# Kernel tuning notes

Hardware: AMD Instinct MI355X
Metric: run time of the kernel (lower is better)

## Reference

```python
import jax, jax.numpy as jnp
import numpy as np
import math

D, DK, DV = 1024, 128, 128
B, S = 4, 2048

def setup_inputs() -> dict:
    key = jax.random.key(0)
    k1, k2, k3, k4 = jax.random.split(key, 4)
    # xavier_normal std = sqrt(2/(fan_in+fan_out))
    std_qk = math.sqrt(2.0 / (D + DK))
    std_v = math.sqrt(2.0 / (D + DV))
    return {
        "X": jax.random.normal(k1, (B, S, D), dtype=jnp.float32),
        "W_q": jax.random.normal(k2, (D, DK), dtype=jnp.float32) * std_qk,
        "W_k": jax.random.normal(k3, (D, DK), dtype=jnp.float32) * std_qk,
        "W_v": jax.random.normal(k4, (D, DV), dtype=jnp.float32) * std_v,
    }

def reference(X, W_q, W_k, W_v):
    # Q,K,V projections: [B,S,D] @ [D,dk] -> [B,S,dk]
    Q = X @ W_q
    K = X @ W_k
    V = X @ W_v
    scale = 1.0 / math.sqrt(DK)
    # NOTE: original torch code calls A.masked_fill(...) without assigning the
    # result, so the causal mask is never actually applied. We replicate the
    # executed math: unmasked scaled dot-product attention.
    A = jnp.einsum("bqd,bkd->bqk", Q, K) * scale  # [B,S,S]
    A = jax.nn.softmax(A, axis=2)
    return jnp.einsum("bqk,bkv->bqv", A, V)  # [B,S,DV]
```

## Files before the change

kernel.cpp:

```cpp
#include <hip/hip_runtime.h>
#include <stdint.h>
#include <math.h>


typedef __attribute__((ext_vector_type(4))) float  f32x4;
typedef __attribute__((ext_vector_type(4))) short  s16x4;
typedef __attribute__((ext_vector_type(8))) short  s16x8;
typedef __attribute__((ext_vector_type(4))) float  fl4;

#define MFMA(a,b,c) __builtin_amdgcn_mfma_f32_16x16x16bf16_1k(a,b,c,0,0,0)

__device__ __forceinline__ short f2bf(float f){
  uint32_t u = __builtin_bit_cast(uint32_t, f);
  u = (u + 0x7FFFu + ((u >> 16) & 1u)) >> 16;
  return (short)u;
}

#define S_LEN   2048
#define D_IN    1024
#define D_HEAD  128
#define NROWS   8192
#define NSPLIT  4
#define KVB     32
#define QBLK    64

#define WT_OFF  0u
#define Q_OFF   786432u
#define K_OFF   (786432u + 2097152u)
#define V_OFF   (786432u + 2u*2097152u)
#define OP_OFF  (786432u + 3u*2097152u)
#define ML_OFF  (OP_OFF + 16777216u)

__global__ __launch_bounds__(256) void wt3_kernel(
    const float* __restrict__ Wq, const float* __restrict__ Wk,
    const float* __restrict__ Wv, short* __restrict__ Wt){
  int i = blockIdx.x * 256 + threadIdx.x;
  int m = i >> 17;
  int r = i & 131071;
  int n = r >> 10;
  int k = r & 1023;
  const float* W = (m == 0) ? Wq : (m == 1 ? Wk : Wv);
  Wt[i] = f2bf(W[k * D_HEAD + n]);
}

__global__ __launch_bounds__(256) void proj_kernel(
    const float* __restrict__ X, const short* __restrict__ Wt,
    short* __restrict__ Qo, short* __restrict__ Ko, short* __restrict__ Vt){
  const int mt  = blockIdx.x;
  const int mat = blockIdx.y;
  const short* Wm = Wt + mat * 131072;

  __shared__ short Xs[64][40];
  __shared__ short Ws[128][40];

  const int tid  = threadIdx.x;
  const int lane = tid & 63;
  const int wid  = tid >> 6;
  const int wm   = (wid >> 1) * 32;
  const int wn   = (wid & 1) * 64;
  const int lr   = lane & 15;
  const int lg   = lane >> 4;

  f32x4 acc[2][4];
  const f32x4 zero4 = {0.f, 0.f, 0.f, 0.f};
  #pragma unroll
  for (int a = 0; a < 2; a++)
    #pragma unroll
    for (int b2 = 0; b2 < 4; b2++) acc[a][b2] = zero4;

  const int xr = tid >> 2;
  const int xc = (tid & 3) * 8;
  const int wr = tid >> 1;
  const int wc = (tid & 1) * 16;

  for (int kt = 0; kt < D_IN; kt += 32){
    __syncthreads();
    {
      const float* src = X + (size_t)(mt * 64 + xr) * D_IN + kt + xc;
      fl4 a0 = *(const fl4*)src;
      fl4 a1 = *(const fl4*)(src + 4);
      s16x8 v;
      #pragma unroll
      for (int j = 0; j < 4; j++){ v[j] = f2bf(a0[j]); v[j+4] = f2bf(a1[j]); }
      *(s16x8*)&Xs[xr][xc] = v;
    }
    {
      const short* src = Wm + (size_t)wr * D_IN + kt + wc;
      s16x8 w0 = *(const s16x8*)src;
      s16x8 w1 = *(const s16x8*)(src + 8);
      *(s16x8*)&Ws[wr][wc]     = w0;
      *(s16x8*)&Ws[wr][wc + 8] = w1;
    }
    __syncthreads();

    #pragma unroll
    for (int kc = 0; kc < 32; kc += 16){
      s16x4 af[2], bf[4];
      #pragma unroll
      for (int mf = 0; mf < 2; mf++)
        af[mf] = *(const s16x4*)&Xs[wm + mf*16 + lr][kc + 4*lg];
      #pragma unroll
      for (int nf = 0; nf < 4; nf++)
        bf[nf] = *(const s16x4*)&Ws[wn + nf*16 + lr][kc + 4*lg];
      #pragma unroll
      for (int mf = 0; mf < 2; mf++)
        #pragma unroll
        for (int nf = 0; nf < 4; nf++)
          acc[mf][nf] = MFMA(af[mf], bf[nf], acc[mf][nf]);
    }
  }

  if (mat < 2){
    short* dst = (mat == 0) ? Qo : Ko;
    #pragma unroll
    for (int mf = 0; mf < 2; mf++)
      #pragma unroll
      for (int nf = 0; nf < 4; nf++)
        #pragma unroll
        for (int r = 0; r < 4; r++){
          int row = mt*64 + wm + mf*16 + 4*lg + r;
          int col = wn + nf*16 + lr;
          dst[(size_t)row * D_HEAD + col] = f2bf(acc[mf][nf][r]);
        }
  } else {
    const int b  = (mt * 64) >> 11;
    const int s0 = (mt * 64) & 2047;
    #pragma unroll
    for (int mf = 0; mf < 2; mf++)
      #pragma unroll
      for (int nf = 0; nf < 4; nf++){
        int dv = wn + nf*16 + lr;
        int s  = s0 + wm + mf*16 + 4*lg;
        s16x4 v;
        #pragma unroll
        for (int r = 0; r < 4; r++) v[r] = f2bf(acc[mf][nf][r]);
        *(s16x4*)&Vt[((size_t)b * D_HEAD + dv) * S_LEN + s] = v;
      }
  }
}

__global__ __launch_bounds__(256) void flash_kernel(
    const short* __restrict__ Q, const short* __restrict__ K,
    const short* __restrict__ Vt, float* __restrict__ Opart,
    float* __restrict__ MLpart){
  const int sp = blockIdx.x;
  const int qt = blockIdx.y;
  const int b  = blockIdx.z;

  __shared__ short Ks[KVB][136];
  __shared__ short Vs[128][40];

  const int tid  = threadIdx.x;
  const int lane = tid & 63;
  const int w    = tid >> 6;
  const int lr   = lane & 15;
  const int lg   = lane >> 4;

  const int qrow = qt * QBLK + w * 16 + lr;
  const short* Qr = Q + (size_t)(b * S_LEN + qrow) * D_HEAD + 4 * lg;
  s16x4 qf[8];
  #pragma unroll
  for (int c = 0; c < 8; c++) qf[c] = *(const s16x4*)(Qr + c * 16);

  const f32x4 zero4 = {0.f, 0.f, 0.f, 0.f};
  f32x4 o[8];
  #pragma unroll
  for (int t = 0; t < 8; t++) o[t] = zero4;
  float m_run = -INFINITY, l_run = 0.0f;

  const int kr = tid >> 3, kc = (tid & 7) * 16;
  const int vr = tid >> 1, vc = (tid & 1) * 16;
  const float scale = 0.08838834764831845f;

  const int kv_beg = sp * (S_LEN / NSPLIT);
  const int kv_end = kv_beg + (S_LEN / NSPLIT);
  for (int kv0 = kv_beg; kv0 < kv_end; kv0 += KVB){
    __syncthreads();
    {
      const short* src = K + (size_t)(b * S_LEN + kv0 + kr) * D_HEAD + kc;
      s16x8 k0 = *(const s16x8*)src;
      s16x8 k1 = *(const s16x8*)(src + 8);
      *(s16x8*)&Ks[kr][kc]     = k0;
      *(s16x8*)&Ks[kr][kc + 8] = k1;
      const short* vsrc = Vt + ((size_t)b * D_HEAD + vr) * S_LEN + kv0 + vc;
      s16x8 v0 = *(const s16x8*)vsrc;
      s16x8 v1 = *(const s16x8*)(vsrc + 8);
      *(s16x8*)&Vs[vr][vc]     = v0;
      *(s16x8*)&Vs[vr][vc + 8] = v1;
    }
    __syncthreads();

    f32x4 sa[2];
    sa[0] = zero4; sa[1] = zero4;
    #pragma unroll
    for (int c = 0; c < 8; c++){
      #pragma unroll
      for (int t = 0; t < 2; t++){
        s16x4 ka = *(const s16x4*)&Ks[t*16 + lr][c*16 + 4*lg];
        sa[t] = MFMA(ka, qf[c], sa[t]);
      }
    }

    float p[8]; float mx = -INFINITY;
    #pragma unroll
    for (int t = 0; t < 2; t++)
      #pragma unroll
      for (int r = 0; r < 4; r++){
        float v = sa[t][r] * scale;
        p[t*4 + r] = v;
        mx = fmaxf(mx, v);
      }
    mx = fmaxf(mx, __shfl_xor(mx, 16));
    mx = fmaxf(mx, __shfl_xor(mx, 32));
    float m_new = fmaxf(m_run, mx);
    float alpha = __expf(m_run - m_new);
    float lsum = 0.0f;
    #pragma unroll
    for (int j = 0; j < 8; j++){ p[j] = __expf(p[j] - m_new); lsum += p[j]; }
    lsum += __shfl_xor(lsum, 16);
    lsum += __shfl_xor(lsum, 32);
    l_run = l_run * alpha + lsum;
    m_run = m_new;

    s16x4 pb0, pb1;
    #pragma unroll
    for (int r = 0; r < 4; r++){ pb0[r] = f2bf(p[r]); pb1[r] = f2bf(p[4 + r]); }
    #pragma unroll
    for (int t = 0; t < 8; t++) o[t] *= alpha;

    #pragma unroll
    for (int dt = 0; dt < 8; dt++){
      s16x4 va0 = *(const s16x4*)&Vs[dt*16 + lr][4*lg];
      s16x4 va1 = *(const s16x4*)&Vs[dt*16 + lr][16 + 4*lg];
      o[dt] = MFMA(va0, pb0, o[dt]);
      o[dt] = MFMA(va1, pb1, o[dt]);
    }
  }

  const size_t grow = (size_t)b * S_LEN + qrow;
  float* Op = Opart + ((size_t)sp * NROWS + grow) * D_HEAD + 4 * lg;
  #pragma unroll
  for (int dt = 0; dt < 8; dt++)
    *(f32x4*)(Op + dt * 16) = o[dt];
  if (lane < 16){
    float* ml = MLpart + ((size_t)sp * NROWS + grow) * 2;
    ml[0] = m_run; ml[1] = l_run;
  }
}

__global__ __launch_bounds__(256) void merge_kernel(
    const float* __restrict__ Opart, const float* __restrict__ MLpart,
    float* __restrict__ out){
  int idx = blockIdx.x * 256 + threadIdx.x;
  int row = idx >> 7;
  float m[NSPLIT], l[NSPLIT];
  float M = -INFINITY;
  #pragma unroll
  for (int s = 0; s < NSPLIT; s++){
    m[s] = MLpart[((size_t)s * NROWS + row) * 2 + 0];
    l[s] = MLpart[((size_t)s * NROWS + row) * 2 + 1];
    M = fmaxf(M, m[s]);
  }
  float L = 0.f, val = 0.f;
  #pragma unroll
  for (int s = 0; s < NSPLIT; s++){
    float e = __expf(m[s] - M);
    L   += l[s] * e;
    val += Opart[(size_t)s * NROWS * D_HEAD + idx] * e;
  }
  out[idx] = val / L;
}

extern "C" void kernel_launch(void* const* d_in, const int* in_sizes, int n_in,
                              void* d_out, int out_size, void* d_ws, size_t ws_size,
                              hipStream_t stream){
  const float* X  = (const float*)d_in[0];
  const float* Wq = (const float*)d_in[1];
  const float* Wk = (const float*)d_in[2];
  const float* Wv = (const float*)d_in[3];
  char* ws = (char*)d_ws;
  short* Wt = (short*)(ws + WT_OFF);
  short* Qp = (short*)(ws + Q_OFF);
  short* Kp = (short*)(ws + K_OFF);
  short* Vt = (short*)(ws + V_OFF);
  float* Op = (float*)(ws + OP_OFF);
  float* Ml = (float*)(ws + ML_OFF);
  float* out = (float*)d_out;

  wt3_kernel  <<<dim3(1536),          dim3(256), 0, stream>>>(Wq, Wk, Wv, Wt);
  proj_kernel <<<dim3(128, 3),        dim3(256), 0, stream>>>(X, Wt, Qp, Kp, Vt);
  flash_kernel<<<dim3(NSPLIT, 32, 4), dim3(256), 0, stream>>>(Qp, Kp, Vt, Op, Ml);
  merge_kernel<<<dim3(4096),          dim3(256), 0, stream>>>(Op, Ml, out);
}
```

Baseline: 152.4 us.

## Use 16x16x32 bf16 MFMA, register prefetch, lazy rescale, folded softmax scale

The projection and attention kernels move to the wider 16x16x32 bf16 MFMA. The projection uses 32-row tiles with a 64-wide k-step, and the launch grid doubles to match. Both kernels prefetch the next K/V or X/W tile into registers while computing on the current one. The softmax scale is folded into W_q during weight conversion. The attention kernel doubles the KV block to 64 and only rescales the running max when it grows by more than 8. Together these aim to cut instruction count, global-load latency stalls and exp/rescale work, at the cost of more registers and LDS per block.

```diff
diff --git a/kernel.cpp b/kernel.cpp
--- a/kernel.cpp
+++ b/kernel.cpp
@@ -8,7 +8,8 @@
 typedef __attribute__((ext_vector_type(8))) short  s16x8;
 typedef __attribute__((ext_vector_type(4))) float  fl4;
 
-#define MFMA(a,b,c) __builtin_amdgcn_mfma_f32_16x16x16bf16_1k(a,b,c,0,0,0)
+#define MFMA16(a,b,c) __builtin_amdgcn_mfma_f32_16x16x16bf16_1k(a,b,c,0,0,0)
+#define MFMA32(a,b,c) __builtin_amdgcn_mfma_f32_16x16x32_bf16(a,b,c,0,0,0)
 
 __device__ __forceinline__ short f2bf(float f){
   uint32_t u = __builtin_bit_cast(uint32_t, f);
@@ -21,8 +22,9 @@
 #define D_HEAD  128
 #define NROWS   8192
 #define NSPLIT  4
-#define KVB     32
-#define QBLK    64
+#define KVB     64
+#define KVPER   (S_LEN / NSPLIT)
+#define NT      (KVPER / KVB)
 
 #define WT_OFF  0u
 #define Q_OFF   786432u
@@ -40,7 +42,9 @@
   int n = r >> 10;
   int k = r & 1023;
   const float* W = (m == 0) ? Wq : (m == 1 ? Wk : Wv);
-  Wt[i] = f2bf(W[k * D_HEAD + n]);
+  float v = W[k * D_HEAD + n];
+  if (m == 0) v *= 0.08838834764831845f;
+  Wt[i] = f2bf(v);
 }
 
 __global__ __launch_bounds__(256) void proj_kernel(
@@ -50,92 +54,91 @@
   const int mat = blockIdx.y;
   const short* Wm = Wt + mat * 131072;
 
-  __shared__ short Xs[64][40];
-  __shared__ short Ws[128][40];
+  __shared__ short Xs[32][72];
+  __shared__ short Ws[128][72];
 
   const int tid  = threadIdx.x;
   const int lane = tid & 63;
   const int wid  = tid >> 6;
-  const int wm   = (wid >> 1) * 32;
+  const int wm   = (wid >> 1) * 16;
   const int wn   = (wid & 1) * 64;
   const int lr   = lane & 15;
-  const int lg   = lane >> 4;
-
-  f32x4 acc[2][4];
+  const int lg8  = (lane >> 4) * 8;
+
   const f32x4 zero4 = {0.f, 0.f, 0.f, 0.f};
-  #pragma unroll
-  for (int a = 0; a < 2; a++)
-    #pragma unroll
-    for (int b2 = 0; b2 < 4; b2++) acc[a][b2] = zero4;
-
-  const int xr = tid >> 2;
-  const int xc = (tid & 3) * 8;
-  const int wr = tid >> 1;
-  const int wc = (tid & 1) * 16;
-
-  for (int kt = 0; kt < D_IN; kt += 32){
+  f32x4 acc[4];
+  #pragma unroll
+  for (int n = 0; n < 4; n++) acc[n] = zero4;
+
+  const int xr = tid >> 3, xc = (tid & 7) * 8;
+  const int wr = tid >> 1, wc = (tid & 1) * 32;
+
+  const float* xsrc0 = X + (size_t)(mt * 32 + xr) * D_IN + xc;
+  const short* wsrc0 = Wm + (size_t)wr * D_IN + wc;
+
+  fl4   xA, xB;
+  s16x8 wR[4];
+
+  xA = *(const fl4*)(xsrc0);
+  xB = *(const fl4*)(xsrc0 + 4);
+  #pragma unroll
+  for (int j = 0; j < 4; j++) wR[j] = *(const s16x8*)(wsrc0 + 8 * j);
+
+  #pragma unroll 1
+  for (int kt = 0; kt < D_IN; kt += 64){
+    {
+      s16x8 v;
+      #pragma unroll
+      for (int j = 0; j < 4; j++){ v[j] = f2bf(xA[j]); v[j+4] = f2bf(xB[j]); }
+      *(s16x8*)&Xs[xr][xc] = v;
+      #pragma unroll
+      for (int j = 0; j < 4; j++) *(s16x8*)&Ws[wr][wc + 8*j] = wR[j];
+    }
     __syncthreads();
-    {
-      const float* src = X + (size_t)(mt * 64 + xr) * D_IN + kt + xc;
-      fl4 a0 = *(const fl4*)src;
-      fl4 a1 = *(const fl4*)(src + 4);
-      s16x8 v;
-      #pragma unroll
-      for (int j = 0; j < 4; j++){ v[j] = f2bf(a0[j]); v[j+4] = f2bf(a1[j]); }
-      *(s16x8*)&Xs[xr][xc] = v;
-    }
-    {
-      const short* src = Wm + (size_t)wr * D_IN + kt + wc;
-      s16x8 w0 = *(const s16x8*)src;
-      s16x8 w1 = *(const s16x8*)(src + 8);
-      *(s16x8*)&Ws[wr][wc]     = w0;
-      *(s16x8*)&Ws[wr][wc + 8] = w1;
+
+    if (kt + 64 < D_IN){
+      xA = *(const fl4*)(xsrc0 + kt + 64);
+      xB = *(const fl4*)(xsrc0 + kt + 68);
+      #pragma unroll
+      for (int j = 0; j < 4; j++) wR[j] = *(const s16x8*)(wsrc0 + kt + 64 + 8*j);
+    }
+
+    #pragma unroll
+    for (int kc = 0; kc < 64; kc += 32){
+      s16x8 af = *(const s16x8*)&Xs[wm + lr][kc + lg8];
+      #pragma unroll
+      for (int n = 0; n < 4; n++){
+        s16x8 bf = *(const s16x8*)&Ws[wn + n*16 + lr][kc + lg8];
+        acc[n] = MFMA32(af, bf, acc[n]);
+      }
     }
     __syncthreads();
-
-    #pragma unroll
-    for (int kc = 0; kc < 32; kc += 16){
-      s16x4 af[2], bf[4];
-      #pragma unroll
-      for (int mf = 0; mf < 2; mf++)
-        af[mf] = *(const s16x4*)&Xs[wm + mf*16 + lr][kc + 4*lg];
-      #pragma unroll
-      for (int nf = 0; nf < 4; nf++)
-        bf[nf] = *(const s16x4*)&Ws[wn + nf*16 + lr][kc + 4*lg];
-      #pragma unroll
-      for (int mf = 0; mf < 2; mf++)
-        #pragma unroll
-        for (int nf = 0; nf < 4; nf++)
-          acc[mf][nf] = MFMA(af[mf], bf[nf], acc[mf][nf]);
-    }
-  }
-
+  }
+
+  const int lg4 = (lane >> 4) * 4;
   if (mat < 2){
     short* dst = (mat == 0) ? Qo : Ko;
     #pragma unroll
-    for (int mf = 0; mf < 2; mf++)
-      #pragma unroll
-      for (int nf = 0; nf < 4; nf++)
-        #pragma unroll
-        for (int r = 0; r < 4; r++){
-          int row = mt*64 + wm + mf*16 + 4*lg + r;
-          int col = wn + nf*16 + lr;
-          dst[(size_t)row * D_HEAD + col] = f2bf(acc[mf][nf][r]);
-        }
+    for (int n = 0; n < 4; n++){
+      int col = wn + n*16 + lr;
+      #pragma unroll
+      for (int r = 0; r < 4; r++){
+        int row = mt*32 + wm + lg4 + r;
+        dst[(size_t)row * D_HEAD + col] = f2bf(acc[n][r]);
+      }
+    }
   } else {
-    const int b  = (mt * 64) >> 11;
-    const int s0 = (mt * 64) & 2047;
-    #pragma unroll
-    for (int mf = 0; mf < 2; mf++)
-      #pragma unroll
-      for (int nf = 0; nf < 4; nf++){
-        int dv = wn + nf*16 + lr;
-        int s  = s0 + wm + mf*16 + 4*lg;
-        s16x4 v;
-        #pragma unroll
-        for (int r = 0; r < 4; r++) v[r] = f2bf(acc[mf][nf][r]);
-        *(s16x4*)&Vt[((size_t)b * D_HEAD + dv) * S_LEN + s] = v;
-      }
+    const int b  = (mt * 32) >> 11;
+    const int s0 = (mt * 32) & 2047;
+    #pragma unroll
+    for (int n = 0; n < 4; n++){
+      int dv = wn + n*16 + lr;
+      int s  = s0 + wm + lg4;
+      s16x4 v;
+      #pragma unroll
+      for (int r = 0; r < 4; r++) v[r] = f2bf(acc[n][r]);
+      *(s16x4*)&Vt[((size_t)b * D_HEAD + dv) * S_LEN + s] = v;
+    }
   }
 }
 
@@ -148,7 +151,7 @@
   const int b  = blockIdx.z;
 
   __shared__ short Ks[KVB][136];
-  __shared__ short Vs[128][40];
+  __shared__ short Vs[128][72];
 
   const int tid  = threadIdx.x;
   const int lane = tid & 63;
@@ -156,11 +159,11 @@
   const int lr   = lane & 15;
   const int lg   = lane >> 4;
 
-  const int qrow = qt * QBLK + w * 16 + lr;
-  const short* Qr = Q + (size_t)(b * S_LEN + qrow) * D_HEAD + 4 * lg;
-  s16x4 qf[8];
-  #pragma unroll
-  for (int c = 0; c < 8; c++) qf[c] = *(const s16x4*)(Qr + c * 16);
+  const int qrow = qt * 64 + w * 16 + lr;
+  const short* Qr = Q + (size_t)(b * S_LEN + qrow) * D_HEAD + 8 * lg;
+  s16x8 qf[4];
+  #pragma unroll
+  for (int c = 0; c < 4; c++) qf[c] = *(const s16x8*)(Qr + c * 32);
 
   const f32x4 zero4 = {0.f, 0.f, 0.f, 0.f};
   f32x4 o[8];
@@ -168,72 +171,103 @@
   for (int t = 0; t < 8; t++) o[t] = zero4;
   float m_run = -INFINITY, l_run = 0.0f;
 
-  const int kr = tid >> 3, kc = (tid & 7) * 16;
-  const int vr = tid >> 1, vc = (tid & 1) * 16;
-  const float scale = 0.08838834764831845f;
-
-  const int kv_beg = sp * (S_LEN / NSPLIT);
-  const int kv_end = kv_beg + (S_LEN / NSPLIT);
-  for (int kv0 = kv_beg; kv0 < kv_end; kv0 += KVB){
-    __syncthreads();
-    {
-      const short* src = K + (size_t)(b * S_LEN + kv0 + kr) * D_HEAD + kc;
-      s16x8 k0 = *(const s16x8*)src;
-      s16x8 k1 = *(const s16x8*)(src + 8);
-      *(s16x8*)&Ks[kr][kc]     = k0;
-      *(s16x8*)&Ks[kr][kc + 8] = k1;
-      const short* vsrc = Vt + ((size_t)b * D_HEAD + vr) * S_LEN + kv0 + vc;
-      s16x8 v0 = *(const s16x8*)vsrc;
-      s16x8 v1 = *(const s16x8*)(vsrc + 8);
-      *(s16x8*)&Vs[vr][vc]     = v0;
-      *(s16x8*)&Vs[vr][vc + 8] = v1;
-    }
-    __syncthreads();
-
-    f32x4 sa[2];
-    sa[0] = zero4; sa[1] = zero4;
-    #pragma unroll
-    for (int c = 0; c < 8; c++){
-      #pragma unroll
-      for (int t = 0; t < 2; t++){
-        s16x4 ka = *(const s16x4*)&Ks[t*16 + lr][c*16 + 4*lg];
-        sa[t] = MFMA(ka, qf[c], sa[t]);
-      }
-    }
-
-    float p[8]; float mx = -INFINITY;
-    #pragma unroll
-    for (int t = 0; t < 2; t++)
+  const short* Kb = K  + (size_t)b * S_LEN * D_HEAD;
+  const short* Vb = Vt + (size_t)b * D_HEAD * S_LEN;
+  const int kr = tid >> 2, kc = (tid & 3) * 32;
+  const int vr = tid >> 1, vc = (tid & 1) * 32;
+
+  s16x8 kR[4], vR[4];
+  const int kv_beg = sp * KVPER;
+
+  {
+    const short* ks = Kb + (size_t)(kv_beg + kr) * D_HEAD + kc;
+    const short* vs = Vb + (size_t)vr * S_LEN + kv_beg + vc;
+    #pragma unroll
+    for (int j = 0; j < 4; j++){
+      kR[j] = *(const s16x8*)(ks + 8*j);
+      vR[j] = *(const s16x8*)(vs + 8*j);
+    }
+  }
+  #pragma unroll
+  for (int j = 0; j < 4; j++){
+    *(s16x8*)&Ks[kr][kc + 8*j] = kR[j];
+    *(s16x8*)&Vs[vr][vc + 8*j] = vR[j];
+  }
+  __syncthreads();
+
+  #pragma unroll 1
+  for (int it = 0; it < NT; ++it){
+    if (it + 1 < NT){
+      int kv0 = kv_beg + (it + 1) * KVB;
+      const short* ks = Kb + (size_t)(kv0 + kr) * D_HEAD + kc;
+      const short* vs = Vb + (size_t)vr * S_LEN + kv0 + vc;
+      #pragma unroll
+      for (int j = 0; j < 4; j++){
+        kR[j] = *(const s16x8*)(ks + 8*j);
+        vR[j] = *(const s16x8*)(vs + 8*j);
+      }
+    }
+
+    f32x4 sa[4];
+    #pragma unroll
+    for (int t = 0; t < 4; t++) sa[t] = zero4;
+    #pragma unroll
+    for (int c = 0; c < 4; c++){
+      #pragma unroll
+      for (int t = 0; t < 4; t++){
+        s16x8 ka = *(const s16x8*)&Ks[t*16 + lr][c*32 + 8*lg];
+        sa[t] = MFMA32(ka, qf[c], sa[t]);
+      }
+    }
+
+    float p[16]; float mx = -INFINITY;
+    #pragma unroll
+    for (int t = 0; t < 4; t++)
       #pragma unroll
       for (int r = 0; r < 4; r++){
-        float v = sa[t][r] * scale;
-        p[t*4 + r] = v;
-        mx = fmaxf(mx, v);
+        p[t*4 + r] = sa[t][r];
+        mx = fmaxf(mx, sa[t][r]);
       }
     mx = fmaxf(mx, __shfl_xor(mx, 16));
     mx = fmaxf(mx, __shfl_xor(mx, 32));
-    float m_new = fmaxf(m_run, mx);
-    float alpha = __expf(m_run - m_new);
+    if (!__all(mx <= m_run + 8.0f)){
+      float m_new = fmaxf(m_run, mx);
+      float alpha = __expf(m_run - m_new);
+      l_run *= alpha;
+      #pragma unroll
+      for (int t = 0; t < 8; t++) o[t] *= alpha;
+      m_run = m_new;
+    }
     float lsum = 0.0f;
     #pragma unroll
-    for (int j = 0; j < 8; j++){ p[j] = __expf(p[j] - m_new); lsum += p[j]; }
+    for (int j = 0; j < 16; j++){ p[j] = __expf(p[j] - m_run); lsum += p[j]; }
     lsum += __shfl_xor(lsum, 16);
     lsum += __shfl_xor(lsum, 32);
-    l_run = l_run * alpha + lsum;
-    m_run = m_new;
-
-    s16x4 pb0, pb1;
-    #pragma unroll
-    for (int r = 0; r < 4; r++){ pb0[r] = f2bf(p[r]); pb1[r] = f2bf(p[4 + r]); }
-    #pragma unroll
-    for (int t = 0; t < 8; t++) o[t] *= alpha;
+    l_run += lsum;
+
+    s16x4 pb[4];
+    #pragma unroll
+    for (int t = 0; t < 4; t++)
+      #pragma unroll
+      for (int r = 0; r < 4; r++) pb[t][r] = f2bf(p[t*4 + r]);
 
     #pragma unroll
     for (int dt = 0; dt < 8; dt++){
-      s16x4 va0 = *(const s16x4*)&Vs[dt*16 + lr][4*lg];
-      s16x4 va1 = *(const s16x4*)&Vs[dt*16 + lr][16 + 4*lg];
-      o[dt] = MFMA(va0, pb0, o[dt]);
-      o[dt] = MFMA(va1, pb1, o[dt]);
+      #pragma unroll
+      for (int t = 0; t < 4; t++){
+        s16x4 va = *(const s16x4*)&Vs[dt*16 + lr][t*16 + 4*lg];
+        o[dt] = MFMA16(va, pb[t], o[dt]);
+      }
+    }
+
+    if (it + 1 < NT){
+      __syncthreads();
+      #pragma unroll
+      for (int j = 0; j < 4; j++){
+        *(s16x8*)&Ks[kr][kc + 8*j] = kR[j];
+        *(s16x8*)&Vs[vr][vc + 8*j] = vR[j];
+      }
+      __syncthreads();
     }
   }
 
@@ -242,7 +276,7 @@
   #pragma unroll
   for (int dt = 0; dt < 8; dt++)
     *(f32x4*)(Op + dt * 16) = o[dt];
-  if (lane < 16){
+  if (lg == 0){
     float* ml = MLpart + ((size_t)sp * NROWS + grow) * 2;
     ml[0] = m_run; ml[1] = l_run;
   }
@@ -288,7 +322,7 @@
   float* out = (float*)d_out;
 
   wt3_kernel  <<<dim3(1536),          dim3(256), 0, stream>>>(Wq, Wk, Wv, Wt);
-  proj_kernel <<<dim3(128, 3),        dim3(256), 0, stream>>>(X, Wt, Qp, Kp, Vt);
+  proj_kernel <<<dim3(256, 3),        dim3(256), 0, stream>>>(X, Wt, Qp, Kp, Vt);
   flash_kernel<<<dim3(NSPLIT, 32, 4), dim3(256), 0, stream>>>(Qp, Kp, Vt, Op, Ml);
   merge_kernel<<<dim3(4096),          dim3(256), 0, stream>>>(Op, Ml, out);
 }
```

New measurement: 128.6 us. 1.19x faster.
